# Performance work log

Hardware: AMD Instinct MI355X
Metric: run time of the kernel (lower is better)

Reference implementation:

```python
import jax, jax.numpy as jnp
import numpy as np

N, E = 50000, 300000
NI, EI, H, OUT, L = 16, 8, 64, 3, 3  # node/edge input widths, hidden, output, conv_depth


def setup_inputs() -> dict:
    key = jax.random.key(0)
    ks = iter(jax.random.split(key, 64))
    def rn(shape, scale=0.05):
        return jax.random.normal(next(ks), shape, dtype=jnp.float32) * scale
    inp = {}
    inp["nodes"] = jax.random.normal(next(ks), (N, NI), dtype=jnp.float32)
    inp["edges"] = jax.random.normal(next(ks), (E, EI), dtype=jnp.float32)
    inp["edge_idx"] = jax.random.randint(next(ks), (E, 2), 0, N, dtype=jnp.int32)
    def mlp_params(prefix, din, lead=None):
        s = () if lead is None else (lead,)
        inp[prefix + "_W1"] = rn(s + (din, H))
        inp[prefix + "_b1"] = jnp.zeros(s + (H,), jnp.float32)
        inp[prefix + "_W2"] = rn(s + (H, H))
        inp[prefix + "_b2"] = jnp.zeros(s + (H,), jnp.float32)
        inp[prefix + "_g"] = jnp.ones(s + (H,), jnp.float32)
        inp[prefix + "_be"] = jnp.zeros(s + (H,), jnp.float32)
    mlp_params("ne", NI)            # node encoder
    mlp_params("ee", EI)            # edge encoder
    mlp_params("nm", 2 * H, lead=L)  # node messengers (stacked over conv_depth)
    mlp_params("em", 3 * H, lead=L)  # edge messengers
    inp["dec_W1"] = rn((H, H)); inp["dec_b1"] = jnp.zeros((H,), jnp.float32)
    inp["dec_W2"] = rn((H, OUT)); inp["dec_b2"] = jnp.zeros((OUT,), jnp.float32)
    return inp


def _lrelu(x):
    return jnp.where(x >= 0, x, 0.05 * x)


def _ln(x, g, b):
    m = jnp.mean(x, axis=-1, keepdims=True)
    v = jnp.mean((x - m) ** 2, axis=-1, keepdims=True)
    return (x - m) * jax.lax.rsqrt(v + 1e-5) * g + b


def _mlp(x, W1, b1, W2, b2, g, b):
    h = _lrelu(x @ W1 + b1)
    h = _lrelu(h @ W2 + b2)
    return _ln(h, g, b)


def reference(nodes, edges, edge_idx,
              ne_W1, ne_b1, ne_W2, ne_b2, ne_g, ne_be,
              ee_W1, ee_b1, ee_W2, ee_b2, ee_g, ee_be,
              nm_W1, nm_b1, nm_W2, nm_b2, nm_g, nm_be,
              em_W1, em_b1, em_W2, em_b2, em_g, em_be,
              dec_W1, dec_b1, dec_W2, dec_b2):
    n = _mlp(nodes, ne_W1, ne_b1, ne_W2, ne_b2, ne_g, ne_be)   # [N, H]
    e = _mlp(edges, ee_W1, ee_b1, ee_W2, ee_b2, ee_g, ee_be)   # [E, H]
    s, r = edge_idx[:, 0], edge_idx[:, 1]
    for i in range(L):
        e = e + _mlp(jnp.concatenate([e, n[s], n[r]], axis=1),
                     em_W1[i], em_b1[i], em_W2[i], em_b2[i], em_g[i], em_be[i])
        aggr = jax.ops.segment_sum(e, s, num_segments=n.shape[0])  # scatter_add onto senders
        n = n + _mlp(jnp.concatenate([n, aggr], axis=1),
                     nm_W1[i], nm_b1[i], nm_W2[i], nm_b2[i], nm_g[i], nm_be[i])
    h = _lrelu(n @ dec_W1 + dec_b1)
    return h @ dec_W2 + dec_b2  # [N, OUT]
```

## Files before the change

### kernel.cpp

```cpp
#include <hip/hip_runtime.h>

typedef __attribute__((ext_vector_type(8))) short short8v;
typedef __attribute__((ext_vector_type(4))) short short4v;
typedef __attribute__((ext_vector_type(4))) float f32x4;

__device__ __forceinline__ float lrelu(float x) { return x >= 0.f ? x : 0.05f * x; }

__device__ __forceinline__ unsigned short bf16_rne(float x) {
    unsigned u = __float_as_uint(x);
    u += 0x7FFFu + ((u >> 16) & 1u);
    return (unsigned short)(u >> 16);
}
__device__ __forceinline__ float bf16_to_f(unsigned short h) {
    return __uint_as_float(((unsigned)h) << 16);
}
__device__ __forceinline__ void split2(float x, unsigned short& hi, unsigned short& lo) {
    hi = bf16_rne(x);
    lo = bf16_rne(x - bf16_to_f(hi));
}


__device__ __forceinline__ void stageW(const float* __restrict__ src, int row0, int nrows,
                                       short* __restrict__ A, int wm, int lane)
{
    #pragma unroll
    for (int it = 0; it < 4; ++it) {
        const int q = it * 64 + lane;
        const int rl = wm * 16 + (q >> 4);
        const int k0 = (q & 15) << 2;
        const int grow = row0 + rl;
        float4 x = (grow < nrows) ? *reinterpret_cast<const float4*>(src + (long long)grow * 64 + k0)
                                  : make_float4(0.f, 0.f, 0.f, 0.f);
        unsigned short h0,h1,h2,h3,l0,l1,l2,l3;
        split2(x.x, h0, l0); split2(x.y, h1, l1); split2(x.z, h2, l2); split2(x.w, h3, l3);
        const int off = rl * 64 + ((((k0 >> 3) ^ (rl & 7))) << 3) + (k0 & 7);
        short4v hv; hv[0]=(short)h0; hv[1]=(short)h1; hv[2]=(short)h2; hv[3]=(short)h3;
        short4v lv; lv[0]=(short)l0; lv[1]=(short)l1; lv[2]=(short)l2; lv[3]=(short)l3;
        *reinterpret_cast<short4v*>(A + off) = hv;
        *reinterpret_cast<short4v*>(A + 4096 + off) = lv;
    }
}

__device__ __forceinline__ void gemm64(const short* __restrict__ A, const short* __restrict__ wf,
                                       int row, int g, int lane, f32x4* __restrict__ acc)
{
    #pragma unroll
    for (int s = 0; s < 2; ++s) {
        const int k8 = s * 4 + g;
        const int aoff = row * 64 + ((k8 ^ (row & 7)) << 3);
        const short8v a_hi = *reinterpret_cast<const short8v*>(A + aoff);
        const short8v a_lo = *reinterpret_cast<const short8v*>(A + 4096 + aoff);
        #pragma unroll
        for (int t = 0; t < 4; ++t) {
            const short8v b_hi = *reinterpret_cast<const short8v*>(wf + ((s*4+t)*2+0)*512 + lane*8);
            const short8v b_lo = *reinterpret_cast<const short8v*>(wf + ((s*4+t)*2+1)*512 + lane*8);
            acc[t] = __builtin_amdgcn_mfma_f32_16x16x32_bf16(a_hi, b_hi, acc[t], 0, 0, 0);
            acc[t] = __builtin_amdgcn_mfma_f32_16x16x32_bf16(a_lo, b_hi, acc[t], 0, 0, 0);
            acc[t] = __builtin_amdgcn_mfma_f32_16x16x32_bf16(a_hi, b_lo, acc[t], 0, 0, 0);
        }
    }
}

__device__ __forceinline__ void repackW(short* __restrict__ A, const float4* __restrict__ q,
                                        int wm, int g, int c4)
{
    #pragma unroll
    for (int r = 0; r < 4; ++r) {
        const int rl = wm * 16 + g * 4 + r;
        const int off = rl * 64 + (((c4 >> 3) ^ (rl & 7)) << 3) + (c4 & 7);
        unsigned short h0,h1,h2,h3,l0,l1,l2,l3;
        split2(q[r].x, h0, l0); split2(q[r].y, h1, l1); split2(q[r].z, h2, l2); split2(q[r].w, h3, l3);
        short4v hv; hv[0]=(short)h0; hv[1]=(short)h1; hv[2]=(short)h2; hv[3]=(short)h3;
        short4v lv; lv[0]=(short)l0; lv[1]=(short)l1; lv[2]=(short)l2; lv[3]=(short)l3;
        *reinterpret_cast<short4v*>(A + off) = hv;
        *reinterpret_cast<short4v*>(A + 4096 + off) = lv;
    }
}

__global__ void k_prepw(const float* __restrict__ emW1, const float* __restrict__ emW2,
                        const float* __restrict__ nmW1, const float* __restrict__ nmW2,
                        const float* __restrict__ eeW2, const float* __restrict__ neW2,
                        const float* __restrict__ decW1,
                        short* __restrict__ wf)
{
    const int cid = blockIdx.x;
    const float* src;
    if (cid < 21) {
        const int layer = cid / 7, j = cid % 7;
        src =
            j == 0 ? emW1 + (size_t)layer * 12288 :
            j == 1 ? emW1 + (size_t)layer * 12288 + 4096 :
            j == 2 ? emW1 + (size_t)layer * 12288 + 8192 :
            j == 3 ? emW2 + (size_t)layer * 4096 :
            j == 4 ? nmW1 + (size_t)layer * 8192 :
            j == 5 ? nmW1 + (size_t)layer * 8192 + 4096 :
                     nmW2 + (size_t)layer * 4096;
    } else {
        src = (cid == 21) ? eeW2 : (cid == 22) ? neW2 : decW1;
    }
    short* dst = wf + (size_t)cid * 8192;
    for (int fr = threadIdx.x; fr < 1024; fr += 256) {
        const int lane = fr & 63;
        const int stp = fr >> 6;
        const int p = stp & 1;
        const int st = stp >> 1;
        const int s = st >> 2, t = st & 3;
        const int col = ((lane & 15) << 2) + t;
        const int k0 = s * 32 + (lane >> 4) * 8;
        short8v o;
        #pragma unroll
        for (int i = 0; i < 8; ++i) {
            const float w = src[(k0 + i) * 64 + col];
            const unsigned short hi = bf16_rne(w);
            o[i] = (short)(p ? bf16_rne(w - bf16_to_f(hi)) : hi);
        }
        *reinterpret_cast<short8v*>(dst + fr * 8) = o;
    }
}

template<int DIN, bool PERM, bool MAKEUV>
__global__ __launch_bounds__(256, 4) void k_enc_mf(
    const float* __restrict__ x, const int* __restrict__ csr,
    const float* __restrict__ W1, const float* __restrict__ b1,
    const short* __restrict__ wfW2, const float* __restrict__ b2,
    const float* __restrict__ gam, const float* __restrict__ bet,
    float* __restrict__ out,
    const short* __restrict__ wfB, const short* __restrict__ wfC,
    float* __restrict__ u, float* __restrict__ v, int nrows)
{
    __shared__ short Hf[8192];
    const int row0 = blockIdx.x * 64;
    const int lane = threadIdx.x & 63;
    const int wm = threadIdx.x >> 6;
    const int g = lane >> 4, c = lane & 15;
    const int c4 = c << 2;
    const int rowA = wm * 16 + c;

    long long orig[4];
    #pragma unroll
    for (int r = 0; r < 4; ++r) {
        const int grow = row0 + wm * 16 + g * 4 + r;
        orig[r] = (grow < nrows) ? (long long)(PERM ? csr[grow] : grow) : -1;
    }

    const f32x4 z4 = {0.f, 0.f, 0.f, 0.f};
    f32x4 acc[4];
    #pragma unroll
    for (int t = 0; t < 4; ++t) acc[t] = z4;

    #pragma unroll
    for (int kq = 0; kq < DIN / 4; ++kq) {
        float xv[4][4];
        #pragma unroll
        for (int r = 0; r < 4; ++r) {
            float4 t4 = make_float4(0.f, 0.f, 0.f, 0.f);
            if (orig[r] >= 0)
                t4 = *reinterpret_cast<const float4*>(x + orig[r] * DIN + kq * 4);
            xv[r][0] = t4.x; xv[r][1] = t4.y; xv[r][2] = t4.z; xv[r][3] = t4.w;
        }
        #pragma unroll
        for (int i = 0; i < 4; ++i) {
            const int k = kq * 4 + i;
            const float4 w4 = *reinterpret_cast<const float4*>(W1 + k * 64 + c4);
            const float wv[4] = {w4.x, w4.y, w4.z, w4.w};
            #pragma unroll
            for (int t = 0; t < 4; ++t)
                #pragma unroll
                for (int r = 0; r < 4; ++r)
                    acc[t][r] = fmaf(xv[r][i], wv[t], acc[t][r]);
        }
    }

    const float4 b1q = *reinterpret_cast<const float4*>(b1 + c4);
    float4 hq[4];
    #pragma unroll
    for (int r = 0; r < 4; ++r) {
        hq[r].x = lrelu(acc[0][r] + b1q.x);
        hq[r].y = lrelu(acc[1][r] + b1q.y);
        hq[r].z = lrelu(acc[2][r] + b1q.z);
        hq[r].w = lrelu(acc[3][r] + b1q.w);
    }
    repackW(Hf, hq, wm, g, c4);
    __builtin_amdgcn_wave_barrier();

    f32x4 acc2[4];
    #pragma unroll
    for (int t = 0; t < 4; ++t) acc2[t] = z4;
    gemm64(Hf, wfW2, rowA, g, lane, acc2);

    const float4 b2q = *reinterpret_cast<const float4*>(b2 + c4);
    const float b2a[4] = {b2q.x, b2q.y, b2q.z, b2q.w};
    #pragma unroll
    for (int t = 0; t < 4; ++t) {
        #pragma unroll
        for (int r = 0; r < 4; ++r) acc2[t][r] = lrelu(acc2[t][r] + b2a[t]);
    }
    const float4 gq = *reinterpret_cast<const float4*>(gam + c4);
    const float4 bq = *reinterpret_cast<const float4*>(bet + c4);
    float4 nq[4];
    #pragma unroll
    for (int r = 0; r < 4; ++r) {
        float s = acc2[0][r] + acc2[1][r] + acc2[2][r] + acc2[3][r];
        s += __shfl_xor(s, 1); s += __shfl_xor(s, 2); s += __shfl_xor(s, 4); s += __shfl_xor(s, 8);
        const float mu = s * 0.015625f;
        float q = 0.f;
        #pragma unroll
        for (int t = 0; t < 4; ++t) { const float d = acc2[t][r] - mu; q = fmaf(d, d, q); }
        q += __shfl_xor(q, 1); q += __shfl_xor(q, 2); q += __shfl_xor(q, 4); q += __shfl_xor(q, 8);
        const float rs = rsqrtf(q * 0.015625f + 1e-5f);
        nq[r].x = (acc2[0][r] - mu) * rs * gq.x + bq.x;
        nq[r].y = (acc2[1][r] - mu) * rs * gq.y + bq.y;
        nq[r].z = (acc2[2][r] - mu) * rs * gq.z + bq.z;
        nq[r].w = (acc2[3][r] - mu) * rs * gq.w + bq.w;
        const int grow = row0 + wm * 16 + g * 4 + r;
        if (grow < nrows)
            *reinterpret_cast<float4*>(out + (long long)grow * 64 + c4) = nq[r];
    }

    if (MAKEUV) {
        repackW(Hf, nq, wm, g, c4);
        __builtin_amdgcn_wave_barrier();
        #pragma unroll
        for (int t = 0; t < 4; ++t) acc2[t] = z4;
        gemm64(Hf, wfB, rowA, g, lane, acc2);
        #pragma unroll
        for (int r = 0; r < 4; ++r) {
            const int grow = row0 + wm * 16 + g * 4 + r;
            if (grow < nrows) {
                float4 o; o.x = acc2[0][r]; o.y = acc2[1][r]; o.z = acc2[2][r]; o.w = acc2[3][r];
                *reinterpret_cast<float4*>(u + (long long)grow * 64 + c4) = o;
            }
        }
        #pragma unroll
        for (int t = 0; t < 4; ++t) acc2[t] = z4;
        gemm64(Hf, wfC, rowA, g, lane, acc2);
        #pragma unroll
        for (int r = 0; r < 4; ++r) {
            const int grow = row0 + wm * 16 + g * 4 + r;
            if (grow < nrows) {
                float4 o; o.x = acc2[0][r]; o.y = acc2[1][r]; o.z = acc2[2][r]; o.w = acc2[3][r];
                *reinterpret_cast<float4*>(v + (long long)grow * 64 + c4) = o;
            }
        }
    }
}

__global__ __launch_bounds__(256, 6) void k_edge_mf(
    float* __restrict__ e, const int* __restrict__ sp, const int* __restrict__ rp,
    const float* __restrict__ u, const float* __restrict__ v,
    const short* __restrict__ wfA, const short* __restrict__ wfW2,
    const float* __restrict__ b1, const float* __restrict__ b2,
    const float* __restrict__ gam, const float* __restrict__ bet, int E)
{
    __shared__ short Ab[8192];
    const int row0 = blockIdx.x * 64;
    const int lane = threadIdx.x & 63;
    const int wm = threadIdx.x >> 6;
    const int g = lane >> 4, c = lane & 15;
    const int c4 = c << 2;
    const int rowA = wm * 16 + c;

    int sidx[4], ridx[4];
    #pragma unroll
    for (int r = 0; r < 4; ++r) {
        const int grow = row0 + wm * 16 + g * 4 + r;
        if (grow < E) { sidx[r] = sp[grow]; ridx[r] = rp[grow]; }
        else          { sidx[r] = 0; ridx[r] = 0; }
    }
    stageW(e, row0, E, Ab, wm, lane);
    __builtin_amdgcn_wave_barrier();
    float4 uu[4], vv[4];
    #pragma unroll
    for (int r = 0; r < 4; ++r) {
        uu[r] = *reinterpret_cast<const float4*>(u + (long long)sidx[r] * 64 + c4);
        vv[r] = *reinterpret_cast<const float4*>(v + (long long)ridx[r] * 64 + c4);
    }

    const f32x4 z4 = {0.f, 0.f, 0.f, 0.f};
    f32x4 acc[4];
    #pragma unroll
    for (int t = 0; t < 4; ++t) acc[t] = z4;
    gemm64(Ab, wfA, rowA, g, lane, acc);

    const float4 b1q = *reinterpret_cast<const float4*>(b1 + c4);
    float4 hq[4];
    #pragma unroll
    for (int r = 0; r < 4; ++r) {
        hq[r].x = lrelu(acc[0][r] + b1q.x + uu[r].x + vv[r].x);
        hq[r].y = lrelu(acc[1][r] + b1q.y + uu[r].y + vv[r].y);
        hq[r].z = lrelu(acc[2][r] + b1q.z + uu[r].z + vv[r].z);
        hq[r].w = lrelu(acc[3][r] + b1q.w + uu[r].w + vv[r].w);
    }
    short4v eh[4], el[4];
    #pragma unroll
    for (int r = 0; r < 4; ++r) {
        const int rl = wm * 16 + g * 4 + r;
        const int off = rl * 64 + (((c4 >> 3) ^ (rl & 7)) << 3) + (c4 & 7);
        eh[r] = *reinterpret_cast<const short4v*>(Ab + off);
        el[r] = *reinterpret_cast<const short4v*>(Ab + 4096 + off);
    }
    __builtin_amdgcn_wave_barrier();
    repackW(Ab, hq, wm, g, c4);
    __builtin_amdgcn_wave_barrier();

    f32x4 acc2[4];
    #pragma unroll
    for (int t = 0; t < 4; ++t) acc2[t] = z4;
    gemm64(Ab, wfW2, rowA, g, lane, acc2);

    const float4 b2q = *reinterpret_cast<const float4*>(b2 + c4);
    const float b2a[4] = {b2q.x, b2q.y, b2q.z, b2q.w};
    #pragma unroll
    for (int t = 0; t < 4; ++t) {
        #pragma unroll
        for (int r = 0; r < 4; ++r) acc2[t][r] = lrelu(acc2[t][r] + b2a[t]);
    }
    const float4 gq = *reinterpret_cast<const float4*>(gam + c4);
    const float4 bq = *reinterpret_cast<const float4*>(bet + c4);
    #pragma unroll
    for (int r = 0; r < 4; ++r) {
        float s = acc2[0][r] + acc2[1][r] + acc2[2][r] + acc2[3][r];
        s += __shfl_xor(s, 1); s += __shfl_xor(s, 2); s += __shfl_xor(s, 4); s += __shfl_xor(s, 8);
        const float mu = s * 0.015625f;
        float q = 0.f;
        #pragma unroll
        for (int t = 0; t < 4; ++t) { const float d = acc2[t][r] - mu; q = fmaf(d, d, q); }
        q += __shfl_xor(q, 1); q += __shfl_xor(q, 2); q += __shfl_xor(q, 4); q += __shfl_xor(q, 8);
        const float rs = rsqrtf(q * 0.015625f + 1e-5f);
        const int grow = row0 + wm * 16 + g * 4 + r;
        if (grow < E) {
            float4 o;
            o.x = (acc2[0][r] - mu) * rs * gq.x + bq.x + bf16_to_f((unsigned short)eh[r][0]) + bf16_to_f((unsigned short)el[r][0]);
            o.y = (acc2[1][r] - mu) * rs * gq.y + bq.y + bf16_to_f((unsigned short)eh[r][1]) + bf16_to_f((unsigned short)el[r][1]);
            o.z = (acc2[2][r] - mu) * rs * gq.z + bq.z + bf16_to_f((unsigned short)eh[r][2]) + bf16_to_f((unsigned short)el[r][2]);
            o.w = (acc2[3][r] - mu) * rs * gq.w + bq.w + bf16_to_f((unsigned short)eh[r][3]) + bf16_to_f((unsigned short)el[r][3]);
            *reinterpret_cast<float4*>(e + (long long)grow * 64 + c4) = o;
        }
    }
}

__global__ __launch_bounds__(256, 4) void k_node_mf(
    float* __restrict__ n, const float* __restrict__ e,
    const int* __restrict__ starts, const int* __restrict__ cnt,
    const short* __restrict__ wfW1a, const short* __restrict__ wfW1b, const short* __restrict__ wfW2,
    const float* __restrict__ b1, const float* __restrict__ b2,
    const float* __restrict__ gam, const float* __restrict__ bet,
    const short* __restrict__ wfB, const short* __restrict__ wfC,
    float* __restrict__ u, float* __restrict__ v, int N)
{
    __shared__ short An[8192];
    __shared__ short Aa[8192];
    const int row0 = blockIdx.x * 64;
    const int lane = threadIdx.x & 63;
    const int wm = threadIdx.x >> 6;
    const int g = lane >> 4, c = lane & 15;
    const int c4 = c << 2;
    const int rowA = wm * 16 + c;

    stageW(n, row0, N, An, wm, lane);

    const int n0 = row0 + wm * 16;
    #pragma unroll 1
    for (int li = 0; li < 16; ++li) {
        const int node = n0 + li;
        float a = 0.f;
        if (node < N) {
            const int st = starts[node];
            const int en = st + cnt[node];
            for (int t = st; t < en; ++t)
                a += e[(long long)t * 64 + lane];
        }
        unsigned short hi, lo; split2(a, hi, lo);
        const int rl = wm * 16 + li;
        const int off = rl * 64 + (((lane >> 3) ^ (rl & 7)) << 3) + (lane & 7);
        Aa[off] = (short)hi;
        Aa[4096 + off] = (short)lo;
    }
    __builtin_amdgcn_wave_barrier();

    const f32x4 z4 = {0.f, 0.f, 0.f, 0.f};
    f32x4 acc[4];
    #pragma unroll
    for (int t = 0; t < 4; ++t) acc[t] = z4;
    gemm64(An, wfW1a, rowA, g, lane, acc);
    gemm64(Aa, wfW1b, rowA, g, lane, acc);

    const float4 b1q = *reinterpret_cast<const float4*>(b1 + c4);
    float4 hq[4];
    #pragma unroll
    for (int r = 0; r < 4; ++r) {
        hq[r].x = lrelu(acc[0][r] + b1q.x);
        hq[r].y = lrelu(acc[1][r] + b1q.y);
        hq[r].z = lrelu(acc[2][r] + b1q.z);
        hq[r].w = lrelu(acc[3][r] + b1q.w);
    }
    __builtin_amdgcn_wave_barrier();
    repackW(Aa, hq, wm, g, c4);
    __builtin_amdgcn_wave_barrier();

    f32x4 acc2[4];
    #pragma unroll
    for (int t = 0; t < 4; ++t) acc2[t] = z4;
    gemm64(Aa, wfW2, rowA, g, lane, acc2);

    const float4 b2q = *reinterpret_cast<const float4*>(b2 + c4);
    const float b2a[4] = {b2q.x, b2q.y, b2q.z, b2q.w};
    #pragma unroll
    for (int t = 0; t < 4; ++t) {
        #pragma unroll
        for (int r = 0; r < 4; ++r) acc2[t][r] = lrelu(acc2[t][r] + b2a[t]);
    }
    const float4 gq = *reinterpret_cast<const float4*>(gam + c4);
    const float4 bq = *reinterpret_cast<const float4*>(bet + c4);
    float4 nq[4];
    #pragma unroll
    for (int r = 0; r < 4; ++r) {
        float s = acc2[0][r] + acc2[1][r] + acc2[2][r] + acc2[3][r];
        s += __shfl_xor(s, 1); s += __shfl_xor(s, 2); s += __shfl_xor(s, 4); s += __shfl_xor(s, 8);
        const float mu = s * 0.015625f;
        float q = 0.f;
        #pragma unroll
        for (int t = 0; t < 4; ++t) { const float d = acc2[t][r] - mu; q = fmaf(d, d, q); }
        q += __shfl_xor(q, 1); q += __shfl_xor(q, 2); q += __shfl_xor(q, 4); q += __shfl_xor(q, 8);
        const float rs = rsqrtf(q * 0.015625f + 1e-5f);
        const int rl = wm * 16 + g * 4 + r;
        const int off = rl * 64 + (((c4 >> 3) ^ (rl & 7)) << 3) + (c4 & 7);
        const short4v nh = *reinterpret_cast<const short4v*>(An + off);
        const short4v nl = *reinterpret_cast<const short4v*>(An + 4096 + off);
        nq[r].x = (acc2[0][r] - mu) * rs * gq.x + bq.x + bf16_to_f((unsigned short)nh[0]) + bf16_to_f((unsigned short)nl[0]);
        nq[r].y = (acc2[1][r] - mu) * rs * gq.y + bq.y + bf16_to_f((unsigned short)nh[1]) + bf16_to_f((unsigned short)nl[1]);
        nq[r].z = (acc2[2][r] - mu) * rs * gq.z + bq.z + bf16_to_f((unsigned short)nh[2]) + bf16_to_f((unsigned short)nl[2]);
        nq[r].w = (acc2[3][r] - mu) * rs * gq.w + bq.w + bf16_to_f((unsigned short)nh[3]) + bf16_to_f((unsigned short)nl[3]);
        const int grow = row0 + rl;
        if (grow < N)
            *reinterpret_cast<float4*>(n + (long long)grow * 64 + c4) = nq[r];
    }

    if (wfB) {
        __builtin_amdgcn_wave_barrier();
        repackW(An, nq, wm, g, c4);
        __builtin_amdgcn_wave_barrier();
        #pragma unroll
        for (int t = 0; t < 4; ++t) acc2[t] = z4;
        gemm64(An, wfB, rowA, g, lane, acc2);
        #pragma unroll
        for (int r = 0; r < 4; ++r) {
            const int grow = row0 + wm * 16 + g * 4 + r;
            if (grow < N) {
                float4 o; o.x = acc2[0][r]; o.y = acc2[1][r]; o.z = acc2[2][r]; o.w = acc2[3][r];
                *reinterpret_cast<float4*>(u + (long long)grow * 64 + c4) = o;
            }
        }
        #pragma unroll
        for (int t = 0; t < 4; ++t) acc2[t] = z4;
        gemm64(An, wfC, rowA, g, lane, acc2);
        #pragma unroll
        for (int r = 0; r < 4; ++r) {
            const int grow = row0 + wm * 16 + g * 4 + r;
            if (grow < N) {
                float4 o; o.x = acc2[0][r]; o.y = acc2[1][r]; o.z = acc2[2][r]; o.w = acc2[3][r];
                *reinterpret_cast<float4*>(v + (long long)grow * 64 + c4) = o;
            }
        }
    }
}

__global__ __launch_bounds__(256, 4) void k_dec_mf(
    const float* __restrict__ n, const short* __restrict__ wfW1, const float* __restrict__ b1,
    const float* __restrict__ W2, const float* __restrict__ b2,
    float* __restrict__ out, int N)
{
    __shared__ short An[8192];
    const int row0 = blockIdx.x * 64;
    const int lane = threadIdx.x & 63;
    const int wm = threadIdx.x >> 6;
    const int g = lane >> 4, c = lane & 15;
    const int c4 = c << 2;
    const int rowA = wm * 16 + c;
    stageW(n, row0, N, An, wm, lane);
    __builtin_amdgcn_wave_barrier();
    const f32x4 z4 = {0.f, 0.f, 0.f, 0.f};
    f32x4 acc[4];
    #pragma unroll
    for (int t = 0; t < 4; ++t) acc[t] = z4;
    gemm64(An, wfW1, rowA, g, lane, acc);
    const float4 b1q = *reinterpret_cast<const float4*>(b1 + c4);
    const float b1a[4] = {b1q.x, b1q.y, b1q.z, b1q.w};
    #pragma unroll
    for (int t = 0; t < 4; ++t)
        #pragma unroll
        for (int r = 0; r < 4; ++r) acc[t][r] = lrelu(acc[t][r] + b1a[t]);
    const float4 w0 = *reinterpret_cast<const float4*>(W2 + c4 * 3);
    const float4 w1 = *reinterpret_cast<const float4*>(W2 + c4 * 3 + 4);
    const float4 w2 = *reinterpret_cast<const float4*>(W2 + c4 * 3 + 8);
    const float wv[12] = {w0.x,w0.y,w0.z,w0.w, w1.x,w1.y,w1.z,w1.w, w2.x,w2.y,w2.z,w2.w};
    float po[4][3];
    #pragma unroll
    for (int r = 0; r < 4; ++r)
        #pragma unroll
        for (int o = 0; o < 3; ++o)
            po[r][o] = acc[0][r]*wv[o] + acc[1][r]*wv[3+o] + acc[2][r]*wv[6+o] + acc[3][r]*wv[9+o];
    #pragma unroll
    for (int m = 1; m <= 8; m <<= 1)
        #pragma unroll
        for (int r = 0; r < 4; ++r)
            #pragma unroll
            for (int o = 0; o < 3; ++o)
                po[r][o] += __shfl_xor(po[r][o], m);
    if (c < 3) {
        #pragma unroll
        for (int r = 0; r < 4; ++r) {
            const int grow = row0 + wm * 16 + g * 4 + r;
            const float val = (c == 0) ? po[r][0] : (c == 1) ? po[r][1] : po[r][2];
            if (grow < N) out[(long long)grow * 3 + c] = b2[c] + val;
        }
    }
}

__global__ void k_hist(const int* __restrict__ eidx, int* __restrict__ cnt, int E)
{
    int i = blockIdx.x * 256 + threadIdx.x;
    if (i < E) atomicAdd(&cnt[eidx[2 * i]], 1);
}

__global__ void k_scan1(const int* __restrict__ cnt, int* __restrict__ starts,
                        int* __restrict__ bsum, int n)
{
    __shared__ int sh[256];
    const int tid = threadIdx.x;
    const int i = blockIdx.x * 256 + tid;
    const int val = (i < n) ? cnt[i] : 0;
    sh[tid] = val; __syncthreads();
    for (int off = 1; off < 256; off <<= 1) {
        int t = (tid >= off) ? sh[tid - off] : 0;
        __syncthreads();
        sh[tid] += t;
        __syncthreads();
    }
    if (i < n) starts[i] = sh[tid] - val;
    if (tid == 255) bsum[blockIdx.x] = sh[255];
}

__global__ void k_scan2(int* __restrict__ bsum, int nb)
{
    __shared__ int sh[256];
    const int tid = threadIdx.x;
    const int val = (tid < nb) ? bsum[tid] : 0;
    sh[tid] = val; __syncthreads();
    for (int off = 1; off < 256; off <<= 1) {
        int t = (tid >= off) ? sh[tid - off] : 0;
        __syncthreads();
        sh[tid] += t;
        __syncthreads();
    }
    if (tid < nb) bsum[tid] = sh[tid] - val;
}

__global__ void k_scan3(int* __restrict__ starts, const int* __restrict__ bsum, int n)
{
    int i = blockIdx.x * 256 + threadIdx.x;
    if (i < n) starts[i] += bsum[blockIdx.x];
}

__global__ void k_scatter(const int* __restrict__ eidx, const int* __restrict__ starts,
                          int* __restrict__ cursor, int* __restrict__ csr,
                          int* __restrict__ sp, int* __restrict__ rp, int E)
{
    int i = blockIdx.x * 256 + threadIdx.x;
    if (i < E) {
        const int s = eidx[2 * i];
        const int p = atomicAdd(&cursor[s], 1);
        const int q = starts[s] + p;
        csr[q] = i;
        sp[q] = s;
        rp[q] = eidx[2 * i + 1];
    }
}

extern "C" void kernel_launch(void* const* d_in, const int* in_sizes, int n_in,
                              void* d_out, int out_size, void* d_ws, size_t ws_size,
                              hipStream_t stream)
{
    (void)in_sizes; (void)n_in; (void)out_size; (void)ws_size;
    constexpr int N = 50000, E = 300000, L = 3;

    const float* nodes = (const float*)d_in[0];
    const float* edges = (const float*)d_in[1];
    const int*   eidx  = (const int*)d_in[2];
    const float* neW1 = (const float*)d_in[3];
    const float* neb1 = (const float*)d_in[4];
    const float* neW2 = (const float*)d_in[5];
    const float* neb2 = (const float*)d_in[6];
    const float* neg  = (const float*)d_in[7];
    const float* nebe = (const float*)d_in[8];
    const float* eeW1 = (const float*)d_in[9];
    const float* eeb1 = (const float*)d_in[10];
    const float* eeW2 = (const float*)d_in[11];
    const float* eeb2 = (const float*)d_in[12];
    const float* eeg  = (const float*)d_in[13];
    const float* eebe = (const float*)d_in[14];
    const float* nmW1 = (const float*)d_in[15];
    const float* nmb1 = (const float*)d_in[16];
    const float* nmW2 = (const float*)d_in[17];
    const float* nmb2 = (const float*)d_in[18];
    const float* nmg  = (const float*)d_in[19];
    const float* nmbe = (const float*)d_in[20];
    const float* emW1 = (const float*)d_in[21];
    const float* emb1 = (const float*)d_in[22];
    const float* emW2 = (const float*)d_in[23];
    const float* emb2 = (const float*)d_in[24];
    const float* emg  = (const float*)d_in[25];
    const float* embe = (const float*)d_in[26];
    const float* decW1 = (const float*)d_in[27];
    const float* decb1 = (const float*)d_in[28];
    const float* decW2 = (const float*)d_in[29];
    const float* decb2 = (const float*)d_in[30];

    float* n   = (float*)d_ws;
    float* u   = n + (size_t)N * 64;
    float* v   = u + (size_t)N * 64;
    float* e   = v + (size_t)N * 64;
    int* cnt    = (int*)(e + (size_t)E * 64);
    int* starts = cnt + N;
    int* csr    = starts + N;
    int* bsum   = csr + E;
    int* cursor = bsum + 256;
    int* sp     = cursor + N;
    int* rp     = sp + E;
    short* wf   = (short*)(rp + E);

    const int nbN = (N + 255) / 256;
    const int nbE = (E + 255) / 256;
    const int nbN64 = (N + 63) / 64;
    const int nbE64 = (E + 63) / 64;

    const short* wfEE  = wf + (size_t)21 * 8192;
    const short* wfNE  = wf + (size_t)22 * 8192;
    const short* wfDec = wf + (size_t)23 * 8192;

    k_prepw<<<24, 256, 0, stream>>>(emW1, emW2, nmW1, nmW2, eeW2, neW2, decW1, wf);
    hipMemsetAsync(cnt, 0, (size_t)N * sizeof(int), stream);
    hipMemsetAsync(cursor, 0, (size_t)N * sizeof(int), stream);
    k_hist<<<nbE, 256, 0, stream>>>(eidx, cnt, E);
    k_scan1<<<nbN, 256, 0, stream>>>(cnt, starts, bsum, N);
    k_scan2<<<1, 256, 0, stream>>>(bsum, nbN);
    k_scan3<<<nbN, 256, 0, stream>>>(starts, bsum, N);
    k_scatter<<<nbE, 256, 0, stream>>>(eidx, starts, cursor, csr, sp, rp, E);

    const short* wl0 = wf;
    k_enc_mf<16, false, true><<<nbN64, 256, 0, stream>>>(
        nodes, nullptr, neW1, neb1, wfNE, neb2, neg, nebe, n,
        wl0 + 8192, wl0 + 2 * 8192, u, v, N);
    k_enc_mf<8, true, false><<<nbE64, 256, 0, stream>>>(
        edges, csr, eeW1, eeb1, wfEE, eeb2, eeg, eebe, e,
        nullptr, nullptr, nullptr, nullptr, E);

    for (int i = 0; i < L; ++i) {
        const short* wl = wf + (size_t)i * 7 * 8192;
        k_edge_mf<<<nbE64, 256, 0, stream>>>(e, sp, rp, u, v, wl, wl + 3 * 8192,
                                             emb1 + i * 64, emb2 + i * 64,
                                             emg + i * 64, embe + i * 64, E);
        const short* wln = (i + 1 < L) ? wf + (size_t)(i + 1) * 7 * 8192 : nullptr;
        k_node_mf<<<nbN64, 256, 0, stream>>>(n, e, starts, cnt,
                                             wl + 4 * 8192, wl + 5 * 8192, wl + 6 * 8192,
                                             nmb1 + i * 64, nmb2 + i * 64,
                                             nmg + i * 64, nmbe + i * 64,
                                             wln ? wln + 8192 : nullptr,
                                             wln ? wln + 2 * 8192 : nullptr,
                                             u, v, N);
    }
    k_dec_mf<<<nbN64, 256, 0, stream>>>(n, wfDec, decb1, decW2, decb2, (float*)d_out, N);
}
```

Measured before the change: 489.8 us.

## Store edge features as bf16 and split aggregation into separate kernel

Edge features are now stored in a single bf16 array instead of fp32, which halves the edge-state traffic read and written by the edge kernel each layer. The edge kernel loads A fragments for the first GEMM directly from global memory and drops the hi/lo split on that operand. The segment-sum moves into a new k_aggr kernel that writes into the u buffer, and the node kernel then stages that buffer like ordinary node features. In exchange the residual edge state loses precision, and each layer pays for one extra kernel launch and an extra pass over the aggregate.

```diff
diff --git a/kernel.cpp b/kernel.cpp
--- a/kernel.cpp
+++ b/kernel.cpp
@@ -20,7 +20,7 @@
 }
 
 
-__device__ __forceinline__ void stageW(const float* __restrict__ src, int row0, int nrows,
+__device__ __forceinline__ void stageW(const float* src, int row0, int nrows,
                                        short* __restrict__ A, int wm, int lane)
 {
     #pragma unroll
@@ -118,7 +118,7 @@
     }
 }
 
-template<int DIN, bool PERM, bool MAKEUV>
+template<int DIN, bool PERM, bool MAKEUV, bool OUTBF16>
 __global__ __launch_bounds__(256, 4) void k_enc_mf(
     const float* __restrict__ x, const int* __restrict__ csr,
     const float* __restrict__ W1, const float* __restrict__ b1,
@@ -213,11 +213,21 @@
         nq[r].z = (acc2[2][r] - mu) * rs * gq.z + bq.z;
         nq[r].w = (acc2[3][r] - mu) * rs * gq.w + bq.w;
         const int grow = row0 + wm * 16 + g * 4 + r;
-        if (grow < nrows)
-            *reinterpret_cast<float4*>(out + (long long)grow * 64 + c4) = nq[r];
-    }
-
-    if (MAKEUV) {
+        if (grow < nrows) {
+            if constexpr (OUTBF16) {
+                short4v st;
+                st[0] = (short)bf16_rne(nq[r].x);
+                st[1] = (short)bf16_rne(nq[r].y);
+                st[2] = (short)bf16_rne(nq[r].z);
+                st[3] = (short)bf16_rne(nq[r].w);
+                *reinterpret_cast<short4v*>(reinterpret_cast<unsigned short*>(out) + (long long)grow * 64 + c4) = st;
+            } else {
+                *reinterpret_cast<float4*>(out + (long long)grow * 64 + c4) = nq[r];
+            }
+        }
+    }
+
+    if constexpr (MAKEUV) {
         repackW(Hf, nq, wm, g, c4);
         __builtin_amdgcn_wave_barrier();
         #pragma unroll
@@ -245,14 +255,14 @@
     }
 }
 
-__global__ __launch_bounds__(256, 6) void k_edge_mf(
-    float* __restrict__ e, const int* __restrict__ sp, const int* __restrict__ rp,
+__global__ __launch_bounds__(256, 4) void k_edge_mf(
+    unsigned short* ebf, const int* __restrict__ sp, const int* __restrict__ rp,
     const float* __restrict__ u, const float* __restrict__ v,
     const short* __restrict__ wfA, const short* __restrict__ wfW2,
     const float* __restrict__ b1, const float* __restrict__ b2,
     const float* __restrict__ gam, const float* __restrict__ bet, int E)
 {
-    __shared__ short Ab[8192];
+    __shared__ short Hf[8192];
     const int row0 = blockIdx.x * 64;
     const int lane = threadIdx.x & 63;
     const int wm = threadIdx.x >> 6;
@@ -267,8 +277,16 @@
         if (grow < E) { sidx[r] = sp[grow]; ridx[r] = rp[grow]; }
         else          { sidx[r] = 0; ridx[r] = 0; }
     }
-    stageW(e, row0, E, Ab, wm, lane);
-    __builtin_amdgcn_wave_barrier();
+    const int arow = (row0 + rowA < E) ? row0 + rowA : 0;
+    const short8v a0 = *reinterpret_cast<const short8v*>(ebf + (long long)arow * 64 + g * 8);
+    const short8v a1 = *reinterpret_cast<const short8v*>(ebf + (long long)arow * 64 + 32 + g * 8);
+    short4v eold[4];
+    #pragma unroll
+    for (int r = 0; r < 4; ++r) {
+        const int grow = row0 + wm * 16 + g * 4 + r;
+        const int rc = (grow < E) ? grow : 0;
+        eold[r] = *reinterpret_cast<const short4v*>(ebf + (long long)rc * 64 + c4);
+    }
     float4 uu[4], vv[4];
     #pragma unroll
     for (int r = 0; r < 4; ++r) {
@@ -280,7 +298,17 @@
     f32x4 acc[4];
     #pragma unroll
     for (int t = 0; t < 4; ++t) acc[t] = z4;
-    gemm64(Ab, wfA, rowA, g, lane, acc);
+    #pragma unroll
+    for (int s = 0; s < 2; ++s) {
+        const short8v a = s ? a1 : a0;
+        #pragma unroll
+        for (int t = 0; t < 4; ++t) {
+            const short8v b_hi = *reinterpret_cast<const short8v*>(wfA + ((s*4+t)*2+0)*512 + lane*8);
+            const short8v b_lo = *reinterpret_cast<const short8v*>(wfA + ((s*4+t)*2+1)*512 + lane*8);
+            acc[t] = __builtin_amdgcn_mfma_f32_16x16x32_bf16(a, b_hi, acc[t], 0, 0, 0);
+            acc[t] = __builtin_amdgcn_mfma_f32_16x16x32_bf16(a, b_lo, acc[t], 0, 0, 0);
+        }
+    }
 
     const float4 b1q = *reinterpret_cast<const float4*>(b1 + c4);
     float4 hq[4];
@@ -291,22 +319,13 @@
         hq[r].z = lrelu(acc[2][r] + b1q.z + uu[r].z + vv[r].z);
         hq[r].w = lrelu(acc[3][r] + b1q.w + uu[r].w + vv[r].w);
     }
-    short4v eh[4], el[4];
-    #pragma unroll
-    for (int r = 0; r < 4; ++r) {
-        const int rl = wm * 16 + g * 4 + r;
-        const int off = rl * 64 + (((c4 >> 3) ^ (rl & 7)) << 3) + (c4 & 7);
-        eh[r] = *reinterpret_cast<const short4v*>(Ab + off);
-        el[r] = *reinterpret_cast<const short4v*>(Ab + 4096 + off);
-    }
+    repackW(Hf, hq, wm, g, c4);
     __builtin_amdgcn_wave_barrier();
-    repackW(Ab, hq, wm, g, c4);
-    __builtin_amdgcn_wave_barrier();
 
     f32x4 acc2[4];
     #pragma unroll
     for (int t = 0; t < 4; ++t) acc2[t] = z4;
-    gemm64(Ab, wfW2, rowA, g, lane, acc2);
+    gemm64(Hf, wfW2, rowA, g, lane, acc2);
 
     const float4 b2q = *reinterpret_cast<const float4*>(b2 + c4);
     const float b2a[4] = {b2q.x, b2q.y, b2q.z, b2q.w};
@@ -329,24 +348,41 @@
         const float rs = rsqrtf(q * 0.015625f + 1e-5f);
         const int grow = row0 + wm * 16 + g * 4 + r;
         if (grow < E) {
-            float4 o;
-            o.x = (acc2[0][r] - mu) * rs * gq.x + bq.x + bf16_to_f((unsigned short)eh[r][0]) + bf16_to_f((unsigned short)el[r][0]);
-            o.y = (acc2[1][r] - mu) * rs * gq.y + bq.y + bf16_to_f((unsigned short)eh[r][1]) + bf16_to_f((unsigned short)el[r][1]);
-            o.z = (acc2[2][r] - mu) * rs * gq.z + bq.z + bf16_to_f((unsigned short)eh[r][2]) + bf16_to_f((unsigned short)el[r][2]);
-            o.w = (acc2[3][r] - mu) * rs * gq.w + bq.w + bf16_to_f((unsigned short)eh[r][3]) + bf16_to_f((unsigned short)el[r][3]);
-            *reinterpret_cast<float4*>(e + (long long)grow * 64 + c4) = o;
-        }
-    }
+            float ox = (acc2[0][r] - mu) * rs * gq.x + bq.x + bf16_to_f((unsigned short)eold[r][0]);
+            float oy = (acc2[1][r] - mu) * rs * gq.y + bq.y + bf16_to_f((unsigned short)eold[r][1]);
+            float oz = (acc2[2][r] - mu) * rs * gq.z + bq.z + bf16_to_f((unsigned short)eold[r][2]);
+            float ow = (acc2[3][r] - mu) * rs * gq.w + bq.w + bf16_to_f((unsigned short)eold[r][3]);
+            short4v st;
+            st[0] = (short)bf16_rne(ox);
+            st[1] = (short)bf16_rne(oy);
+            st[2] = (short)bf16_rne(oz);
+            st[3] = (short)bf16_rne(ow);
+            *reinterpret_cast<short4v*>(ebf + (long long)grow * 64 + c4) = st;
+        }
+    }
+}
+
+__global__ __launch_bounds__(256) void k_aggr(
+    const unsigned short* __restrict__ ebf, const int* __restrict__ starts,
+    const int* __restrict__ cnt, float* __restrict__ aggr, int N)
+{
+    const int node = blockIdx.x * 4 + (threadIdx.x >> 6);
+    if (node >= N) return;
+    const int j = threadIdx.x & 63;
+    const int st = starts[node], en = st + cnt[node];
+    float a = 0.f;
+    for (int t = st; t < en; ++t)
+        a += bf16_to_f(ebf[(long long)t * 64 + j]);
+    aggr[(long long)node * 64 + j] = a;
 }
 
 __global__ __launch_bounds__(256, 4) void k_node_mf(
-    float* __restrict__ n, const float* __restrict__ e,
-    const int* __restrict__ starts, const int* __restrict__ cnt,
+    float* n, const float* aggr,
     const short* __restrict__ wfW1a, const short* __restrict__ wfW1b, const short* __restrict__ wfW2,
     const float* __restrict__ b1, const float* __restrict__ b2,
     const float* __restrict__ gam, const float* __restrict__ bet,
     const short* __restrict__ wfB, const short* __restrict__ wfC,
-    float* __restrict__ u, float* __restrict__ v, int N)
+    float* u, float* v, int N)
 {
     __shared__ short An[8192];
     __shared__ short Aa[8192];
@@ -358,24 +394,7 @@
     const int rowA = wm * 16 + c;
 
     stageW(n, row0, N, An, wm, lane);
-
-    const int n0 = row0 + wm * 16;
-    #pragma unroll 1
-    for (int li = 0; li < 16; ++li) {
-        const int node = n0 + li;
-        float a = 0.f;
-        if (node < N) {
-            const int st = starts[node];
-            const int en = st + cnt[node];
-            for (int t = st; t < en; ++t)
-                a += e[(long long)t * 64 + lane];
-        }
-        unsigned short hi, lo; split2(a, hi, lo);
-        const int rl = wm * 16 + li;
-        const int off = rl * 64 + (((lane >> 3) ^ (rl & 7)) << 3) + (lane & 7);
-        Aa[off] = (short)hi;
-        Aa[4096 + off] = (short)lo;
-    }
+    stageW(aggr, row0, N, Aa, wm, lane);
     __builtin_amdgcn_wave_barrier();
 
     const f32x4 z4 = {0.f, 0.f, 0.f, 0.f};
@@ -619,8 +638,7 @@
     float* n   = (float*)d_ws;
     float* u   = n + (size_t)N * 64;
     float* v   = u + (size_t)N * 64;
-    float* e   = v + (size_t)N * 64;
-    int* cnt    = (int*)(e + (size_t)E * 64);
+    int* cnt    = (int*)(v + (size_t)N * 64);
     int* starts = cnt + N;
     int* csr    = starts + N;
     int* bsum   = csr + E;
@@ -628,6 +646,7 @@
     int* sp     = cursor + N;
     int* rp     = sp + E;
     short* wf   = (short*)(rp + E);
+    unsigned short* ebf = (unsigned short*)(wf + (size_t)24 * 8192);
 
     const int nbN = (N + 255) / 256;
     const int nbE = (E + 255) / 256;
@@ -648,20 +667,21 @@
     k_scatter<<<nbE, 256, 0, stream>>>(eidx, starts, cursor, csr, sp, rp, E);
 
     const short* wl0 = wf;
-    k_enc_mf<16, false, true><<<nbN64, 256, 0, stream>>>(
+    k_enc_mf<16, false, true, false><<<nbN64, 256, 0, stream>>>(
         nodes, nullptr, neW1, neb1, wfNE, neb2, neg, nebe, n,
         wl0 + 8192, wl0 + 2 * 8192, u, v, N);
-    k_enc_mf<8, true, false><<<nbE64, 256, 0, stream>>>(
-        edges, csr, eeW1, eeb1, wfEE, eeb2, eeg, eebe, e,
+    k_enc_mf<8, true, false, true><<<nbE64, 256, 0, stream>>>(
+        edges, csr, eeW1, eeb1, wfEE, eeb2, eeg, eebe, (float*)ebf,
         nullptr, nullptr, nullptr, nullptr, E);
 
     for (int i = 0; i < L; ++i) {
         const short* wl = wf + (size_t)i * 7 * 8192;
-        k_edge_mf<<<nbE64, 256, 0, stream>>>(e, sp, rp, u, v, wl, wl + 3 * 8192,
+        k_edge_mf<<<nbE64, 256, 0, stream>>>(ebf, sp, rp, u, v, wl, wl + 3 * 8192,
                                              emb1 + i * 64, emb2 + i * 64,
                                              emg + i * 64, embe + i * 64, E);
+        k_aggr<<<(N + 3) / 4, 256, 0, stream>>>(ebf, starts, cnt, u, N);
         const short* wln = (i + 1 < L) ? wf + (size_t)(i + 1) * 7 * 8192 : nullptr;
-        k_node_mf<<<nbN64, 256, 0, stream>>>(n, e, starts, cnt,
+        k_node_mf<<<nbN64, 256, 0, stream>>>(n, u,
                                              wl + 4 * 8192, wl + 5 * 8192, wl + 6 * 8192,
                                              nmb1 + i * 64, nmb2 + i * 64,
                                              nmg + i * 64, nmbe + i * 64,
```

After: 425.6 us. 1.15x faster.
